# Optimization experiments

Hardware: AMD Instinct MI355X
Metric: run time of the kernel (lower is better)

The kernel has to match this reference:

```python
import jax, jax.numpy as jnp
import numpy as np

B, N, DIM = 4, 2048, 512
H, DH = 8, 64  # heads, dim_head; inner_dim = H*DH = 512
SCALE = DH ** -0.5
EPS = 1e-5


def _layer_norm(x, gamma):
    # LayerNorm with learned gamma and beta fixed to zeros (beta is a buffer)
    mu = jnp.mean(x, axis=-1, keepdims=True)
    var = jnp.var(x, axis=-1, keepdims=True)
    return (x - mu) * jax.lax.rsqrt(var + EPS) * gamma


def setup_inputs() -> dict:
    key = jax.random.key(0)
    ks = jax.random.split(key, 6)
    x = jax.random.normal(ks[0], (B, N, DIM), jnp.float32)
    mask = jax.random.bernoulli(ks[1], 0.9, (B, N))  # bool [b, n]
    gamma = jnp.ones((DIM,), jnp.float32)            # pre-attn LayerNorm gamma
    Wq = jax.random.normal(ks[2], (DIM, H * DH), jnp.float32) * 0.02
    Wkv = jax.random.normal(ks[3], (DIM, 2 * DH), jnp.float32) * 0.02  # shared single KV head (MQA)
    null_kv = jax.random.normal(ks[4], (2, DH), jnp.float32)
    Wout = jax.random.normal(ks[5], (H * DH, DIM), jnp.float32) * 0.02
    out_gamma = jnp.ones((DIM,), jnp.float32)        # post-proj LayerNorm gamma
    return {"x": x, "mask": mask, "gamma": gamma, "Wq": Wq, "Wkv": Wkv,
            "null_kv": null_kv, "Wout": Wout, "out_gamma": out_gamma}


def reference(x, mask, gamma, Wq, Wkv, null_kv, Wout, out_gamma):
    b, n, _ = x.shape
    xn = _layer_norm(x, gamma)
    # queries: per-head; keys/values: single shared head (multi-query)
    q = (xn @ Wq).reshape(b, n, H, DH).transpose(0, 2, 1, 3) * SCALE  # [b,h,n,d]
    kv = xn @ Wkv                                                     # [b,n,2d]
    k, v = kv[..., :DH], kv[..., DH:]                                 # [b,n,d]
    # prepend learned null key/value (attention sink) shared across batch
    nk = jnp.broadcast_to(null_kv[0], (b, 1, DH))
    nv = jnp.broadcast_to(null_kv[1], (b, 1, DH))
    k = jnp.concatenate([nk, k], axis=1)  # [b, n+1, d]
    v = jnp.concatenate([nv, v], axis=1)
    sim = jnp.einsum('bhid,bjd->bhij', q, k)  # [b,h,n,n+1]
    # mask padded with True for the null token, broadcast over heads/queries
    m = jnp.concatenate([jnp.ones((b, 1), bool), mask], axis=1)
    max_neg = -jnp.finfo(sim.dtype).max
    sim = jnp.where(m[:, None, None, :], sim, max_neg)
    attn = jax.nn.softmax(sim.astype(jnp.float32), axis=-1).astype(x.dtype)
    out = jnp.einsum('bhij,bjd->bhid', attn, v)       # [b,h,n,d]
    out = out.transpose(0, 2, 1, 3).reshape(b, n, H * DH)
    return _layer_norm(out @ Wout, out_gamma)
```

## Files before the change

### kernel.cpp

```cpp
#include <hip/hip_runtime.h>

typedef __attribute__((ext_vector_type(8)))  short bf16x8;
typedef __attribute__((ext_vector_type(4)))  float f32x4;
typedef __attribute__((ext_vector_type(16))) float f32x16;
typedef __attribute__((ext_vector_type(4)))  unsigned u32x4;

#define Nx 2048
#define CTXx 2049
#define KCAP 2112
#define QSCALE 0.18033688f

__device__ __forceinline__ short f2bs(float x){
    unsigned u = __builtin_bit_cast(unsigned, x);
    u = (u + 0x7fffu + ((u >> 16) & 1u)) >> 16;
    return (short)u;
}
__device__ __forceinline__ unsigned pack_trunc(float a, float b){
    return __builtin_amdgcn_perm(__builtin_bit_cast(unsigned, b),
                                 __builtin_bit_cast(unsigned, a), 0x07060302u);
}

__global__ void __launch_bounds__(256) ln1_prep_kernel(const float* __restrict__ x,
                                                       const float* __restrict__ g,
                                                       short* __restrict__ xnb,
                                                       const float* __restrict__ Wq,
                                                       const float* __restrict__ Wkv,
                                                       const float* __restrict__ Wout,
                                                       const float* __restrict__ nkv,
                                                       const int* __restrict__ mask,
                                                       short* __restrict__ WcatT,
                                                       short* __restrict__ WoutT,
                                                       short* __restrict__ kb,
                                                       short* __restrict__ vbt,
                                                       short* __restrict__ mvb){
    __shared__ float ls[64][65];
    int t = threadIdx.x;
    if (blockIdx.x < 2048){
        int w = t >> 6, lane = t & 63;
        size_t row = (size_t)blockIdx.x * 4 + w;
        const float* xr = x + row * 512 + lane * 8;
        float4 a = *(const float4*)xr;
        float4 b = *(const float4*)(xr + 4);
        float s = a.x + a.y + a.z + a.w + b.x + b.y + b.z + b.w;
        float q = a.x*a.x + a.y*a.y + a.z*a.z + a.w*a.w
                + b.x*b.x + b.y*b.y + b.z*b.z + b.w*b.w;
        #pragma unroll
        for (int m = 1; m < 64; m <<= 1){ s += __shfl_xor(s, m, 64); q += __shfl_xor(q, m, 64); }
        float mu  = s * (1.f / 512.f);
        float var = fmaxf(q * (1.f / 512.f) - mu * mu, 0.f);
        float r   = rsqrtf(var + 1e-5f);
        const float* gr = g + lane * 8;
        float4 g0 = *(const float4*)gr;
        float4 g1 = *(const float4*)(gr + 4);
        bf16x8 o;
        o[0] = f2bs((a.x - mu) * r * g0.x); o[1] = f2bs((a.y - mu) * r * g0.y);
        o[2] = f2bs((a.z - mu) * r * g0.z); o[3] = f2bs((a.w - mu) * r * g0.w);
        o[4] = f2bs((b.x - mu) * r * g1.x); o[5] = f2bs((b.y - mu) * r * g1.y);
        o[6] = f2bs((b.z - mu) * r * g1.z); o[7] = f2bs((b.w - mu) * r * g1.w);
        *(bf16x8*)(xnb + row * 512 + lane * 8) = o;
        return;
    }
    int bid = blockIdx.x - 2048;
    if (bid == 144){
        int b = t >> 6, d = t & 63;
        kb[((size_t)b * KCAP) * 64 + d] = f2bs(nkv[d]);
        vbt[((size_t)b * 64 + d) * KCAP + 0] = f2bs(nkv[64 + d]);
        return;
    }
    if (bid == 145){
        int b = t >> 6, i6 = t & 63;
        if (i6 < 63){
            short* kr = kb + ((size_t)b * KCAP + 2049 + i6) * 64;
            #pragma unroll
            for (int d = 0; d < 64; d += 8) *(int4*)(kr + d) = make_int4(0, 0, 0, 0);
        }
        {
            short* vr = vbt + ((size_t)b * 64 + i6) * KCAP;
            for (int k = 2049; k < KCAP; k++) vr[k] = 0;
        }
        int lane = t & 63;
        int s = lane >> 4, hb = (lane >> 3) & 1, j = lane & 7;
        int g = (j < 4) ? ((2 * s) & 3) : ((2 * s + 1) & 3);
        int kl = (s >> 1) * 32 + 8 * g + 4 * hb + (j & 3);
        const int* mrow = mask + b * Nx;
        for (int wi = 0; wi < 33; wi++){
            int gk = wi * 64 + kl;
            int ok = (gk == 0) ? 1 : ((gk <= Nx) ? mrow[gk - 1] : 0);
            mvb[(size_t)b * 2112 + wi * 64 + lane] = ok ? (short)0x3F80 : (short)0;
        }
        return;
    }
    bool isOut = (bid >= 80);
    int b2 = isOut ? bid - 80 : bid;
    int ntile = isOut ? (b2 & 7) : (b2 % 10);
    int ktile = isOut ? (b2 >> 3) : (b2 / 10);
    int n0 = ntile * 64, k0 = ktile * 64;
    #pragma unroll
    for (int rr = 0; rr < 64; rr += 16){
        int r = rr + (t >> 4), c = (t & 15) * 4;
        float4 v;
        if (isOut)            v = *(const float4*)(Wout + (size_t)(k0 + r) * 512 + n0 + c);
        else if (n0 < 512)    v = *(const float4*)(Wq   + (size_t)(k0 + r) * 512 + n0 + c);
        else                  v = *(const float4*)(Wkv  + (size_t)(k0 + r) * 128 + (n0 - 512) + c);
        ls[c + 0][r] = v.x; ls[c + 1][r] = v.y; ls[c + 2][r] = v.z; ls[c + 3][r] = v.w;
    }
    __syncthreads();
    int rn = t >> 2, kc = (t & 3) * 16;
    short tmp[16];
    #pragma unroll
    for (int j = 0; j < 16; j++) tmp[j] = f2bs(ls[rn][kc + j]);
    short* dst = (isOut ? WoutT : WcatT) + (size_t)(n0 + rn) * 512 + k0 + kc;
    *(int4*)dst       = *(int4*)&tmp[0];
    *(int4*)(dst + 8) = *(int4*)&tmp[8];
}

__global__ void __launch_bounds__(256) ln2_kernel(const float* __restrict__ z,
                                                  const float* __restrict__ g,
                                                  float* __restrict__ out){
    int w = threadIdx.x >> 6, lane = threadIdx.x & 63;
    size_t row = (size_t)blockIdx.x * 4 + w;
    const float* xr = z + row * 512 + lane * 8;
    float4 a = *(const float4*)xr;
    float4 b = *(const float4*)(xr + 4);
    float s = a.x + a.y + a.z + a.w + b.x + b.y + b.z + b.w;
    float q = a.x*a.x + a.y*a.y + a.z*a.z + a.w*a.w
            + b.x*b.x + b.y*b.y + b.z*b.z + b.w*b.w;
    #pragma unroll
    for (int m = 1; m < 64; m <<= 1){ s += __shfl_xor(s, m, 64); q += __shfl_xor(q, m, 64); }
    float mu  = s * (1.f / 512.f);
    float var = fmaxf(q * (1.f / 512.f) - mu * mu, 0.f);
    float r   = rsqrtf(var + 1e-5f);
    const float* gr = g + lane * 8;
    float4 g0 = *(const float4*)gr;
    float4 g1 = *(const float4*)(gr + 4);
    float4 o0, o1;
    o0.x = (a.x - mu) * r * g0.x; o0.y = (a.y - mu) * r * g0.y;
    o0.z = (a.z - mu) * r * g0.z; o0.w = (a.w - mu) * r * g0.w;
    o1.x = (b.x - mu) * r * g1.x; o1.y = (b.y - mu) * r * g1.y;
    o1.z = (b.z - mu) * r * g1.z; o1.w = (b.w - mu) * r * g1.w;
    float* op = out + row * 512 + lane * 8;
    *(float4*)op = o0; *(float4*)(op + 4) = o1;
}

__global__ void __launch_bounds__(256, 1) gemm_qkv(const short* __restrict__ A,
                                                   const short* __restrict__ BwT,
                                                   const int* __restrict__ mask,
                                                   short* __restrict__ qb,
                                                   short* __restrict__ kb,
                                                   short* __restrict__ vbt){
    __shared__ short As[2][128][72];
    __shared__ short Bs[2][160][72];
    int t = threadIdx.x;
    int lane = t & 63, w = t >> 6;
    int l16 = lane & 15, quad = lane >> 4;
    int wm = w & 1, wn = w >> 1;
    int row0 = blockIdx.y * 128, col0 = blockIdx.x * 160;
    f32x4 acc[4][5];
    #pragma unroll
    for (int i = 0; i < 4; i++)
        #pragma unroll
        for (int j = 0; j < 5; j++) acc[i][j] = (f32x4){0.f, 0.f, 0.f, 0.f};
    int ar = t >> 1, ak = (t & 1) * 32;
    const short* ap = A + (size_t)(row0 + ar) * 512 + ak;
    int4 a0 = *(const int4*)(ap);      int4 a1 = *(const int4*)(ap + 8);
    int4 a2 = *(const int4*)(ap + 16); int4 a3 = *(const int4*)(ap + 24);
    int4 pb[5];
    int brow[5], bseg[5];
    #pragma unroll
    for (int ps = 0; ps < 5; ps++){
        int idx = ps * 256 + t;
        brow[ps] = idx >> 3; bseg[ps] = (idx & 7) * 8;
        pb[ps] = *(const int4*)(BwT + (size_t)(col0 + brow[ps]) * 512 + bseg[ps]);
    }
    int p = 0;
    for (int k0 = 0; k0 < 512; k0 += 64){
        *(int4*)&As[p][ar][ak]      = a0;
        *(int4*)&As[p][ar][ak + 8]  = a1;
        *(int4*)&As[p][ar][ak + 16] = a2;
        *(int4*)&As[p][ar][ak + 24] = a3;
        #pragma unroll
        for (int ps = 0; ps < 5; ps++)
            *(int4*)&Bs[p][brow[ps]][bseg[ps]] = pb[ps];
        __syncthreads();
        int kn = k0 + 64;
        if (kn < 512){
            a0 = *(const int4*)(ap + kn);      a1 = *(const int4*)(ap + kn + 8);
            a2 = *(const int4*)(ap + kn + 16); a3 = *(const int4*)(ap + kn + 24);
            #pragma unroll
            for (int ps = 0; ps < 5; ps++)
                pb[ps] = *(const int4*)(BwT + (size_t)(col0 + brow[ps]) * 512 + kn + bseg[ps]);
        }
        #pragma unroll
        for (int ks = 0; ks < 2; ks++){
            bf16x8 af[4], bfr[5];
            #pragma unroll
            for (int mt = 0; mt < 4; mt++)
                af[mt] = *(const bf16x8*)&As[p][wm * 64 + mt * 16 + l16][ks * 32 + quad * 8];
            #pragma unroll
            for (int nt = 0; nt < 5; nt++)
                bfr[nt] = *(const bf16x8*)&Bs[p][wn * 80 + nt * 16 + l16][ks * 32 + quad * 8];
            #pragma unroll
            for (int mt = 0; mt < 4; mt++)
                #pragma unroll
                for (int nt = 0; nt < 5; nt++)
                    acc[mt][nt] = __builtin_amdgcn_mfma_f32_16x16x32_bf16(af[mt], bfr[nt], acc[mt][nt], 0, 0, 0);
        }
        p ^= 1;
    }
    #pragma unroll
    for (int mt = 0; mt < 4; mt++)
        #pragma unroll
        for (int nt = 0; nt < 5; nt++)
            #pragma unroll
            for (int r = 0; r < 4; r++){
                int row = row0 + wm * 64 + mt * 16 + quad * 4 + r;
                int col = col0 + wn * 80 + nt * 16 + l16;
                float v = acc[mt][nt][r];
                int bb = row >> 11, ii = row & 2047;
                if (col < 512){
                    qb[(size_t)row * 512 + col] = f2bs(v * QSCALE);
                } else if (col < 576){
                    kb[((size_t)bb * KCAP + ii + 1) * 64 + (col - 512)] = f2bs(v);
                } else {
                    if (!mask[bb * Nx + ii]) v = 0.f;
                    vbt[((size_t)bb * 64 + (col - 576)) * KCAP + ii + 1] = f2bs(v);
                }
            }
}

__global__ void __launch_bounds__(256, 2) gemm_out(const short* __restrict__ A,
                                                   const short* __restrict__ BwT,
                                                   float* __restrict__ C){
    __shared__ short As[2][128][72];
    __shared__ short Bs[2][128][72];
    int t = threadIdx.x;
    int lane = t & 63, w = t >> 6;
    int l16 = lane & 15, quad = lane >> 4;
    int wm = w & 1, wn = w >> 1;
    int row0 = blockIdx.y * 128, col0 = blockIdx.x * 128;
    f32x4 acc[4][4];
    #pragma unroll
    for (int i = 0; i < 4; i++)
        #pragma unroll
        for (int j = 0; j < 4; j++) acc[i][j] = (f32x4){0.f, 0.f, 0.f, 0.f};
    int ar = t >> 1, ak = (t & 1) * 32;
    const short* ap = A   + (size_t)(row0 + ar) * 512 + ak;
    const short* bp = BwT + (size_t)(col0 + ar) * 512 + ak;
    int4 a0 = *(const int4*)(ap);      int4 a1 = *(const int4*)(ap + 8);
    int4 a2 = *(const int4*)(ap + 16); int4 a3 = *(const int4*)(ap + 24);
    int4 b0 = *(const int4*)(bp);      int4 b1 = *(const int4*)(bp + 8);
    int4 b2 = *(const int4*)(bp + 16); int4 b3 = *(const int4*)(bp + 24);
    int p = 0;
    for (int k0 = 0; k0 < 512; k0 += 64){
        *(int4*)&As[p][ar][ak]      = a0;
        *(int4*)&As[p][ar][ak + 8]  = a1;
        *(int4*)&As[p][ar][ak + 16] = a2;
        *(int4*)&As[p][ar][ak + 24] = a3;
        *(int4*)&Bs[p][ar][ak]      = b0;
        *(int4*)&Bs[p][ar][ak + 8]  = b1;
        *(int4*)&Bs[p][ar][ak + 16] = b2;
        *(int4*)&Bs[p][ar][ak + 24] = b3;
        __syncthreads();
        int kn = k0 + 64;
        if (kn < 512){
            a0 = *(const int4*)(ap + kn);      a1 = *(const int4*)(ap + kn + 8);
            a2 = *(const int4*)(ap + kn + 16); a3 = *(const int4*)(ap + kn + 24);
            b0 = *(const int4*)(bp + kn);      b1 = *(const int4*)(bp + kn + 8);
            b2 = *(const int4*)(bp + kn + 16); b3 = *(const int4*)(bp + kn + 24);
        }
        #pragma unroll
        for (int ks = 0; ks < 2; ks++){
            bf16x8 af[4], bfr[4];
            #pragma unroll
            for (int mt = 0; mt < 4; mt++)
                af[mt] = *(const bf16x8*)&As[p][wm * 64 + mt * 16 + l16][ks * 32 + quad * 8];
            #pragma unroll
            for (int nt = 0; nt < 4; nt++)
                bfr[nt] = *(const bf16x8*)&Bs[p][wn * 64 + nt * 16 + l16][ks * 32 + quad * 8];
            #pragma unroll
            for (int mt = 0; mt < 4; mt++)
                #pragma unroll
                for (int nt = 0; nt < 4; nt++)
                    acc[mt][nt] = __builtin_amdgcn_mfma_f32_16x16x32_bf16(af[mt], bfr[nt], acc[mt][nt], 0, 0, 0);
        }
        p ^= 1;
    }
    #pragma unroll
    for (int mt = 0; mt < 4; mt++)
        #pragma unroll
        for (int nt = 0; nt < 4; nt++)
            #pragma unroll
            for (int r = 0; r < 4; r++){
                int row = row0 + wm * 64 + mt * 16 + quad * 4 + r;
                int col = col0 + wn * 64 + nt * 16 + l16;
                C[(size_t)row * 512 + col] = acc[mt][nt][r];
            }
}

__global__ void __launch_bounds__(256, 2) attn_kernel(const short* __restrict__ qb,
                                                      const short* __restrict__ kb,
                                                      const short* __restrict__ vbt,
                                                      const short* __restrict__ mvb,
                                                      short* __restrict__ ob){
    __shared__ short Ks[2][64][72];
    __shared__ short Vt[2][64][72];
    int t = threadIdx.x;
    int lane = t & 63, w = t >> 6;
    int n32 = lane & 31, hb = lane >> 5;
    int b = blockIdx.y, i0 = blockIdx.x * 16;
    int head = 2 * w + (n32 >> 4), row = i0 + (n32 & 15);
    bf16x8 qf[4];
    {
        const short* qp = qb + ((size_t)(b * Nx + row)) * 512 + head * 64 + hb * 8;
        #pragma unroll
        for (int ks = 0; ks < 4; ks++) qf[ks] = *(const bf16x8*)(qp + ks * 16);
    }
    f32x16 oacc[2], lacc;
    #pragma unroll
    for (int j = 0; j < 16; j++){ oacc[0][j] = 0.f; oacc[1][j] = 0.f; lacc[j] = 0.f; }

    int skey = t >> 2, sd = (t & 3) * 16;
    int vd   = t >> 2, vk = (t & 3) * 16;
    const short* kgp = kb  + (size_t)b * KCAP * 64 + skey * 64 + sd;
    const short* vgp = vbt + ((size_t)b * 64 + vd) * KCAP + vk;
    const short* mvq = mvb + (size_t)b * 2112 + hb * 8;

    int off = (blockIdx.x + 8 * blockIdx.y) % 33;

    int jt = off;
    int4 pk0 = *(const int4*)(kgp + (size_t)jt * 4096);
    int4 pk1 = *(const int4*)(kgp + (size_t)jt * 4096 + 8);
    int4 pv0 = *(const int4*)(vgp + jt * 64);
    int4 pv1 = *(const int4*)(vgp + jt * 64 + 8);

    int p = 0;
    for (int it = 0; it < 33; ++it){
        *(int4*)&Ks[p][skey][sd]     = pk0;
        *(int4*)&Ks[p][skey][sd + 8] = pk1;
        *(int4*)&Vt[p][vd][vk]       = make_int4(pv0.x, pv0.y, pv1.x, pv1.y);
        *(int4*)&Vt[p][vd][vk + 8]   = make_int4(pv0.z, pv0.w, pv1.z, pv1.w);
        __syncthreads();
        bf16x8 mvf[4];
        #pragma unroll
        for (int s = 0; s < 4; s++) mvf[s] = *(const bf16x8*)(mvq + jt * 64 + s * 16);
        int jn = jt + 1; if (jn == 33) jn = 0;
        if (it + 1 < 33){
            pk0 = *(const int4*)(kgp + (size_t)jn * 4096);
            pk1 = *(const int4*)(kgp + (size_t)jn * 4096 + 8);
            pv0 = *(const int4*)(vgp + jn * 64);
            pv1 = *(const int4*)(vgp + jn * 64 + 8);
        }
        f32x16 sf[2];
        #pragma unroll
        for (int i = 0; i < 2; i++)
            #pragma unroll
            for (int j = 0; j < 16; j++) sf[i][j] = 0.f;
        __builtin_amdgcn_s_setprio(1);
        #pragma unroll
        for (int ks = 0; ks < 4; ks++){
            #pragma unroll
            for (int kt = 0; kt < 2; kt++){
                bf16x8 kf = *(const bf16x8*)&Ks[p][kt * 32 + n32][ks * 16 + hb * 8];
                sf[kt] = __builtin_amdgcn_mfma_f32_32x32x16_bf16(kf, qf[ks], sf[kt], 0, 0, 0);
            }
        }
        __builtin_amdgcn_s_setprio(0);
        unsigned pg[8][2];
        #pragma unroll
        for (int kt = 0; kt < 2; kt++){
            #pragma unroll
            for (int g4 = 0; g4 < 4; g4++){
                float pr[4];
                #pragma unroll
                for (int tt = 0; tt < 4; tt++)
                    pr[tt] = __builtin_amdgcn_exp2f(sf[kt][g4 * 4 + tt]);
                pg[kt * 4 + g4][0] = pack_trunc(pr[0], pr[1]);
                pg[kt * 4 + g4][1] = pack_trunc(pr[2], pr[3]);
            }
        }
        __builtin_amdgcn_s_setprio(1);
        #pragma unroll
        for (int s = 0; s < 4; s++){
            bf16x8 pa = __builtin_bit_cast(bf16x8,
                (u32x4){pg[2 * s][0], pg[2 * s][1], pg[2 * s + 1][0], pg[2 * s + 1][1]});
            lacc = __builtin_amdgcn_mfma_f32_32x32x16_bf16(pa, mvf[s], lacc, 0, 0, 0);
            #pragma unroll
            for (int nt = 0; nt < 2; nt++){
                bf16x8 vf = *(const bf16x8*)&Vt[p][nt * 32 + n32][s * 16 + hb * 8];
                oacc[nt] = __builtin_amdgcn_mfma_f32_32x32x16_bf16(pa, vf, oacc[nt], 0, 0, 0);
            }
        }
        __builtin_amdgcn_s_setprio(0);
        p ^= 1;
        jt = jn;
    }
    #pragma unroll
    for (int r = 0; r < 16; r++){
        float linv = 1.f / lacc[r];
        int hr = (r & 3) + 8 * (r >> 2) + 4 * hb;
        int grow = i0 + (hr & 15);
        int ghead = 2 * w + (hr >> 4);
        short* op = ob + ((size_t)(b * Nx + grow)) * 512 + ghead * 64 + n32;
        op[0]  = f2bs(oacc[0][r] * linv);
        op[32] = f2bs(oacc[1][r] * linv);
    }
}

extern "C" void kernel_launch(void* const* d_in, const int* in_sizes, int n_in,
                              void* d_out, int out_size, void* d_ws, size_t ws_size,
                              hipStream_t stream){
    const float* x     = (const float*)d_in[0];
    const int*   mask  = (const int*)  d_in[1];
    const float* gamma = (const float*)d_in[2];
    const float* Wq    = (const float*)d_in[3];
    const float* Wkv   = (const float*)d_in[4];
    const float* nkv   = (const float*)d_in[5];
    const float* Wout  = (const float*)d_in[6];
    const float* og    = (const float*)d_in[7];
    float* out = (float*)d_out;

    short* xnb   = (short*)d_ws;
    short* qb    = xnb + (size_t)4194304;
    short* kb    = qb  + (size_t)4194304;
    short* vbt   = kb  + (size_t)540672;
    short* ob    = vbt + (size_t)540672;
    short* WcatT = ob  + (size_t)4194304;
    short* WoutT = WcatT + (size_t)327680;
    short* mvb   = WoutT + (size_t)262144;
    float* zb    = (float*)d_ws;

    ln1_prep_kernel<<<2194, 256, 0, stream>>>(x, gamma, xnb, Wq, Wkv, Wout, nkv, mask,
                                              WcatT, WoutT, kb, vbt, mvb);
    gemm_qkv    <<<dim3(4, 64), 256, 0, stream>>>(xnb, WcatT, mask, qb, kb, vbt);
    attn_kernel <<<dim3(128, 4), 256, 0, stream>>>(qb, kb, vbt, mvb, ob);
    gemm_out    <<<dim3(4, 64), 256, 0, stream>>>(ob, WoutT, zb);
    ln2_kernel  <<<2048, 256, 0, stream>>>(zb, og, out);
}
```

Measured before the change: 199.8 us.

## Split attention key range across two wave groups per block and merge partials

Doubles the attention block to 512 threads, with two halves of four waves each. Each half processes 17 of 34 key tiles, so the key capacity is padded from 33 to 34 tiles. Partial numerators and denominators are combined through shared memory at the end. This split-K approach cuts the serial loop length per block and raises the wave count to hide latency, at the cost of extra padded work, a reduction step, and more register and LDS pressure.

```diff
diff --git a/kernel.cpp b/kernel.cpp
--- a/kernel.cpp
+++ b/kernel.cpp
@@ -7,7 +7,8 @@
 
 #define Nx 2048
 #define CTXx 2049
-#define KCAP 2112
+#define KCAP 2176
+#define NTILES 34
 #define QSCALE 0.18033688f
 
 __device__ __forceinline__ short f2bs(float x){
@@ -69,8 +70,8 @@
     }
     if (bid == 145){
         int b = t >> 6, i6 = t & 63;
-        if (i6 < 63){
-            short* kr = kb + ((size_t)b * KCAP + 2049 + i6) * 64;
+        for (int rr = 2049 + i6; rr < KCAP; rr += 64){
+            short* kr = kb + ((size_t)b * KCAP + rr) * 64;
             #pragma unroll
             for (int d = 0; d < 64; d += 8) *(int4*)(kr + d) = make_int4(0, 0, 0, 0);
         }
@@ -83,10 +84,10 @@
         int g = (j < 4) ? ((2 * s) & 3) : ((2 * s + 1) & 3);
         int kl = (s >> 1) * 32 + 8 * g + 4 * hb + (j & 3);
         const int* mrow = mask + b * Nx;
-        for (int wi = 0; wi < 33; wi++){
+        for (int wi = 0; wi < NTILES; wi++){
             int gk = wi * 64 + kl;
             int ok = (gk == 0) ? 1 : ((gk <= Nx) ? mrow[gk - 1] : 0);
-            mvb[(size_t)b * 2112 + wi * 64 + lane] = ok ? (short)0x3F80 : (short)0;
+            mvb[(size_t)b * KCAP + wi * 64 + lane] = ok ? (short)0x3F80 : (short)0;
         }
         return;
     }
@@ -297,18 +298,18 @@
             }
 }
 
-__global__ void __launch_bounds__(256, 2) attn_kernel(const short* __restrict__ qb,
+__global__ void __launch_bounds__(512, 4) attn_kernel(const short* __restrict__ qb,
                                                       const short* __restrict__ kb,
                                                       const short* __restrict__ vbt,
                                                       const short* __restrict__ mvb,
                                                       short* __restrict__ ob){
-    __shared__ short Ks[2][64][72];
-    __shared__ short Vt[2][64][72];
+    __shared__ short smem[36864];
     int t = threadIdx.x;
     int lane = t & 63, w = t >> 6;
+    int half = w >> 2, w4 = w & 3;
     int n32 = lane & 31, hb = lane >> 5;
     int b = blockIdx.y, i0 = blockIdx.x * 16;
-    int head = 2 * w + (n32 >> 4), row = i0 + (n32 & 15);
+    int head = 2 * w4 + (n32 >> 4), row = i0 + (n32 & 15);
     bf16x8 qf[4];
     {
         const short* qp = qb + ((size_t)(b * Nx + row)) * 512 + head * 64 + hb * 8;
@@ -319,37 +320,40 @@
     #pragma unroll
     for (int j = 0; j < 16; j++){ oacc[0][j] = 0.f; oacc[1][j] = 0.f; lacc[j] = 0.f; }
 
-    int skey = t >> 2, sd = (t & 3) * 16;
-    int vd   = t >> 2, vk = (t & 3) * 16;
+    int th = t & 255;
+    int skey = th >> 2, sd = (th & 3) * 16;
+    int vd   = th >> 2, vk = (th & 3) * 16;
+    short* Kb = smem +         (half * 2) * 4608;
+    short* Vb = smem + 18432 + (half * 2) * 4608;
     const short* kgp = kb  + (size_t)b * KCAP * 64 + skey * 64 + sd;
     const short* vgp = vbt + ((size_t)b * 64 + vd) * KCAP + vk;
-    const short* mvq = mvb + (size_t)b * 2112 + hb * 8;
-
-    int off = (blockIdx.x + 8 * blockIdx.y) % 33;
-
-    int jt = off;
+    const short* mvq = mvb + (size_t)b * KCAP + hb * 8;
+
+    int off = (blockIdx.x + 8 * blockIdx.y) % NTILES;
+    int jt = off + (half ? 17 : 0); if (jt >= NTILES) jt -= NTILES;
+
     int4 pk0 = *(const int4*)(kgp + (size_t)jt * 4096);
     int4 pk1 = *(const int4*)(kgp + (size_t)jt * 4096 + 8);
     int4 pv0 = *(const int4*)(vgp + jt * 64);
     int4 pv1 = *(const int4*)(vgp + jt * 64 + 8);
 
     int p = 0;
-    for (int it = 0; it < 33; ++it){
-        *(int4*)&Ks[p][skey][sd]     = pk0;
-        *(int4*)&Ks[p][skey][sd + 8] = pk1;
-        *(int4*)&Vt[p][vd][vk]       = make_int4(pv0.x, pv0.y, pv1.x, pv1.y);
-        *(int4*)&Vt[p][vd][vk + 8]   = make_int4(pv0.z, pv0.w, pv1.z, pv1.w);
+    for (int it = 0; it < 17; ++it){
+        short* Ksp = Kb + p * 4608;
+        short* Vtp = Vb + p * 4608;
+        *(int4*)&Ksp[skey * 72 + sd]     = pk0;
+        *(int4*)&Ksp[skey * 72 + sd + 8] = pk1;
+        *(int4*)&Vtp[vd * 72 + vk]       = make_int4(pv0.x, pv0.y, pv1.x, pv1.y);
+        *(int4*)&Vtp[vd * 72 + vk + 8]   = make_int4(pv0.z, pv0.w, pv1.z, pv1.w);
         __syncthreads();
         bf16x8 mvf[4];
         #pragma unroll
         for (int s = 0; s < 4; s++) mvf[s] = *(const bf16x8*)(mvq + jt * 64 + s * 16);
-        int jn = jt + 1; if (jn == 33) jn = 0;
-        if (it + 1 < 33){
-            pk0 = *(const int4*)(kgp + (size_t)jn * 4096);
-            pk1 = *(const int4*)(kgp + (size_t)jn * 4096 + 8);
-            pv0 = *(const int4*)(vgp + jn * 64);
-            pv1 = *(const int4*)(vgp + jn * 64 + 8);
-        }
+        int jn = jt + 1; if (jn == NTILES) jn = 0;
+        pk0 = *(const int4*)(kgp + (size_t)jn * 4096);
+        pk1 = *(const int4*)(kgp + (size_t)jn * 4096 + 8);
+        pv0 = *(const int4*)(vgp + jn * 64);
+        pv1 = *(const int4*)(vgp + jn * 64 + 8);
         f32x16 sf[2];
         #pragma unroll
         for (int i = 0; i < 2; i++)
@@ -360,7 +364,7 @@
         for (int ks = 0; ks < 4; ks++){
             #pragma unroll
             for (int kt = 0; kt < 2; kt++){
-                bf16x8 kf = *(const bf16x8*)&Ks[p][kt * 32 + n32][ks * 16 + hb * 8];
+                bf16x8 kf = *(const bf16x8*)&Ksp[(kt * 32 + n32) * 72 + ks * 16 + hb * 8];
                 sf[kt] = __builtin_amdgcn_mfma_f32_32x32x16_bf16(kf, qf[ks], sf[kt], 0, 0, 0);
             }
         }
@@ -386,7 +390,7 @@
             lacc = __builtin_amdgcn_mfma_f32_32x32x16_bf16(pa, mvf[s], lacc, 0, 0, 0);
             #pragma unroll
             for (int nt = 0; nt < 2; nt++){
-                bf16x8 vf = *(const bf16x8*)&Vt[p][nt * 32 + n32][s * 16 + hb * 8];
+                bf16x8 vf = *(const bf16x8*)&Vtp[(nt * 32 + n32) * 72 + s * 16 + hb * 8];
                 oacc[nt] = __builtin_amdgcn_mfma_f32_32x32x16_bf16(pa, vf, oacc[nt], 0, 0, 0);
             }
         }
@@ -394,15 +398,35 @@
         p ^= 1;
         jt = jn;
     }
-    #pragma unroll
-    for (int r = 0; r < 16; r++){
-        float linv = 1.f / lacc[r];
-        int hr = (r & 3) + 8 * (r >> 2) + 4 * hb;
-        int grow = i0 + (hr & 15);
-        int ghead = 2 * w + (hr >> 4);
-        short* op = ob + ((size_t)(b * Nx + grow)) * 512 + ghead * 64 + n32;
-        op[0]  = f2bs(oacc[0][r] * linv);
-        op[32] = f2bs(oacc[1][r] * linv);
+    __syncthreads();
+    float* cm = (float*)smem;
+    int base = (w4 * 64 + lane) * 49;
+    if (half){
+        #pragma unroll
+        for (int r = 0; r < 16; r++){
+            cm[base + r]      = lacc[r];
+            cm[base + 16 + r] = oacc[0][r];
+            cm[base + 32 + r] = oacc[1][r];
+        }
+    }
+    __syncthreads();
+    if (!half){
+        #pragma unroll
+        for (int r = 0; r < 16; r++){
+            lacc[r]    += cm[base + r];
+            oacc[0][r] += cm[base + 16 + r];
+            oacc[1][r] += cm[base + 32 + r];
+        }
+        #pragma unroll
+        for (int r = 0; r < 16; r++){
+            float linv = 1.f / lacc[r];
+            int hr = (r & 3) + 8 * (r >> 2) + 4 * hb;
+            int grow = i0 + (hr & 15);
+            int ghead = 2 * w4 + (hr >> 4);
+            short* op = ob + ((size_t)(b * Nx + grow)) * 512 + ghead * 64 + n32;
+            op[0]  = f2bs(oacc[0][r] * linv);
+            op[32] = f2bs(oacc[1][r] * linv);
+        }
     }
 }
 
@@ -422,8 +446,8 @@
     short* xnb   = (short*)d_ws;
     short* qb    = xnb + (size_t)4194304;
     short* kb    = qb  + (size_t)4194304;
-    short* vbt   = kb  + (size_t)540672;
-    short* ob    = vbt + (size_t)540672;
+    short* vbt   = kb  + (size_t)557056;
+    short* ob    = vbt + (size_t)557056;
     short* WcatT = ob  + (size_t)4194304;
     short* WoutT = WcatT + (size_t)327680;
     short* mvb   = WoutT + (size_t)262144;
@@ -432,7 +456,7 @@
     ln1_prep_kernel<<<2194, 256, 0, stream>>>(x, gamma, xnb, Wq, Wkv, Wout, nkv, mask,
                                               WcatT, WoutT, kb, vbt, mvb);
     gemm_qkv    <<<dim3(4, 64), 256, 0, stream>>>(xnb, WcatT, mask, qb, kb, vbt);
-    attn_kernel <<<dim3(128, 4), 256, 0, stream>>>(qb, kb, vbt, mvb, ob);
+    attn_kernel <<<dim3(128, 4), 512, 0, stream>>>(qb, kb, vbt, mvb, ob);
     gemm_out    <<<dim3(4, 64), 256, 0, stream>>>(ob, WoutT, zb);
     ln2_kernel  <<<2048, 256, 0, stream>>>(zb, og, out);
 }
```

New measurement: 239.0 us. +19.6%, slower.
